# Kernel tuning notes

Measured on AMD Instinct MI355X. Metric: run time of the kernel, lower is better.

The kernel has to match this reference:

```python
import jax, jax.numpy as jnp
import numpy as np

N_NODES = 100000


def _gcn_layer(h_in, W, b, src, dst, norm, num_nodes):
    # PyG GCNConv: linear transform first, then normalized scatter-add aggregation
    h = h_in @ W                                   # [N, out_dim]
    msg = h[src] * norm[:, None]                   # gather + scale over edges
    out = jax.ops.segment_sum(msg, dst, num_segments=num_nodes)
    return out + b


def setup_inputs() -> dict:
    key = jax.random.key(0)
    k1, k2, k3, k4, k5 = jax.random.split(key, 5)
    d_in, d_hid, d_out = 128, 128, 128
    x = jax.random.normal(k1, (N_NODES, d_in), dtype=jnp.float32)
    edge_index = jax.random.randint(k2, (2, 1600000), 0, N_NODES, dtype=jnp.int64)
    # Glorot-ish init for weights, zeros for bias (as in GCNConv defaults)
    W1 = jax.random.normal(k3, (d_in, d_hid), dtype=jnp.float32) / np.sqrt(d_in)
    b1 = jnp.zeros((d_hid,), dtype=jnp.float32)
    W2 = jax.random.normal(k4, (d_hid, d_out), dtype=jnp.float32) / np.sqrt(d_hid)
    b2 = jnp.zeros((d_out,), dtype=jnp.float32)
    return {"x": x, "edge_index": edge_index, "W1": W1, "b1": b1, "W2": W2, "b2": b2}


def reference(x, edge_index, W1, b1, W2, b2):
    num_nodes = x.shape[0]
    # Add self-loops (GCNConv default add_self_loops=True)
    loop = jnp.arange(num_nodes, dtype=edge_index.dtype)
    src = jnp.concatenate([edge_index[0], loop])
    dst = jnp.concatenate([edge_index[1], loop])
    # Symmetric normalization: deg^{-1/2}[src] * deg^{-1/2}[dst]
    deg = jax.ops.segment_sum(jnp.ones_like(dst, dtype=x.dtype), dst, num_segments=num_nodes)
    dinv = jnp.where(deg > 0, jax.lax.rsqrt(deg), 0.0)
    norm = dinv[src] * dinv[dst]                   # [E + N]

    h = _gcn_layer(x, W1, b1, src, dst, norm, num_nodes)
    h = jax.nn.relu(h)                             # dropout is identity in eval mode
    out = _gcn_layer(h, W2, b2, src, dst, norm, num_nodes)
    return out
```

## Files before the change

### kernel.cpp

```cpp
#include <hip/hip_runtime.h>


#define DIM 128
#define CAP 192
typedef unsigned short ushort_t;
typedef unsigned int uint_t;
typedef __attribute__((ext_vector_type(8))) short bf16x8;
typedef __attribute__((ext_vector_type(4))) float f32x4;
typedef __attribute__((ext_vector_type(2))) float f32x2;
typedef __attribute__((ext_vector_type(2))) unsigned int u32x2;

static __device__ __forceinline__ uint_t f2bf(float f) {
    union { float f; uint_t u; } c; c.f = f;
    uint_t u = c.u;
    return (u + 0x7FFFu + ((u >> 16) & 1u)) >> 16;
}
static __device__ __forceinline__ float bf2f(uint_t h) {
    union { uint_t u; float f; } c; c.u = h << 16;
    return c.f;
}
static __device__ __forceinline__ float as_f(uint_t u) {
    union { uint_t u; float f; } c; c.u = u;
    return c.f;
}
static __device__ __forceinline__ void gld16(const void* g, void* l) {
    __builtin_amdgcn_global_load_lds(
        (const __attribute__((address_space(1))) uint_t*)g,
        (__attribute__((address_space(3))) uint_t*)l, 16, 0, 0);
}

__global__ __launch_bounds__(256) void k_bin(const int* __restrict__ src,
                                             const int* __restrict__ dst,
                                             int* __restrict__ bcur,
                                             uint_t* __restrict__ stage,
                                             int E, int RB) {
    int e = blockIdx.x * 256 + threadIdx.x;
    if (e >= E) return;
    int slice = blockIdx.x & 31;
    int s = src[e], d = dst[e];
    int idx = slice * RB + (d >> 7);
    int c = atomicAdd(&bcur[idx], 1);
    if (c < CAP)
        stage[(size_t)idx * CAP + c] = (uint_t)((s << 7) | (d & 127));
}

__global__ __launch_bounds__(1024) void k_bscan(const int* __restrict__ bcur,
                                                int* __restrict__ bbase, int RB) {
    __shared__ int sdat[1024];
    int t = threadIdx.x;
    int v = 0;
    if (t < RB)
        #pragma unroll
        for (int s = 0; s < 32; ++s) v += min(bcur[s * RB + t], CAP);
    sdat[t] = v;
    __syncthreads();
    #pragma unroll
    for (int o = 1; o < 1024; o <<= 1) {
        int x = (t >= o) ? sdat[t - o] : 0;
        __syncthreads();
        sdat[t] += x;
        __syncthreads();
    }
    if (t < RB) bbase[t] = sdat[t] - v;
}

__global__ __launch_bounds__(256) void k_build(const uint_t* __restrict__ stage,
                                               const int* __restrict__ bcur,
                                               const int* __restrict__ bbase,
                                               int* __restrict__ off,
                                               float* __restrict__ dinv,
                                               int* __restrict__ csr_src,
                                               int RB, int N, int E) {
    __shared__ int scnt[33];
    __shared__ int cnt[128], excl[128], lcur[128];
    __shared__ uint_t ent[32 * CAP];
    int b = blockIdx.x, t = threadIdx.x;
    if (t < 32) scnt[t + 1] = min(bcur[t * RB + b], CAP);
    if (t == 0) scnt[0] = 0;
    if (t < 128) { cnt[t] = 0; lcur[t] = 0; }
    __syncthreads();
    if (t == 0)
        for (int s = 1; s <= 32; ++s) scnt[s] += scnt[s - 1];
    __syncthreads();
    int total = scnt[32];
    for (int s = 0; s < 32; ++s) {
        int c0 = scnt[s], c1 = scnt[s + 1];
        const uint_t* sp = stage + (size_t)(s * RB + b) * CAP - c0;
        for (int i = c0 + t; i < c1; i += 256) ent[i] = sp[i];
    }
    __syncthreads();
    for (int i = t; i < total; i += 256) atomicAdd(&cnt[ent[i] & 127], 1);
    __syncthreads();
    if (t < 128) excl[t] = cnt[t];
    __syncthreads();
    #pragma unroll
    for (int o = 1; o < 128; o <<= 1) {
        int x = 0;
        if (t < 128 && t >= o) x = excl[t - o];
        __syncthreads();
        if (t < 128) excl[t] += x;
        __syncthreads();
    }
    int base = bbase[b];
    if (t < 128) {
        excl[t] -= cnt[t];
        int node = (b << 7) + t;
        if (node < N) {
            off[node] = base + excl[t];
            dinv[node] = rsqrtf((float)cnt[t] + 1.0f);
        }
    }
    if (b == RB - 1 && t == 0) off[N] = E;
    __syncthreads();
    for (int i = t; i < total; i += 256) {
        uint_t v = ent[i];
        int dl = v & 127;
        int pos = base + excl[dl] + atomicAdd(&lcur[dl], 1);
        csr_src[pos] = (int)(v >> 7);
    }
}

__global__ __launch_bounds__(256) void k_prep(const float* __restrict__ W1,
                                              const float* __restrict__ W2,
                                              const float* __restrict__ x,
                                              short* __restrict__ whi,
                                              short* __restrict__ wlo,
                                              short* __restrict__ xhi,
                                              short* __restrict__ xlo,
                                              int N, int nxc) {
    int t = threadIdx.x;
    if (blockIdx.x < 16) {
        int g = blockIdx.x * 256 + t;
        int layer = g >> 11, c = g & 2047;
        const float* W = layer ? W2 : W1;
        int ks = c >> 9, nt = (c >> 6) & 7, l = c & 63;
        int q = l >> 4, m = l & 15;
        int n = nt * 16 + m;
        bf16x8 h8, l8;
        #pragma unroll
        for (int j = 0; j < 8; ++j) {
            int k = ks * 32 + q * 8 + j;
            float f = W[k * 128 + n];
            uint_t hb = f2bf(f);
            h8[j] = (short)hb;
            l8[j] = (short)f2bf(f - bf2f(hb));
        }
        ((bf16x8*)whi)[g] = h8;
        ((bf16x8*)wlo)[g] = l8;
    } else {
        int c = (blockIdx.x - 16) * 256 + t;
        if (c >= nxc) return;
        int rb = c >> 11, row = (c >> 4) & 127, cc = c & 15;
        int node = rb * 128 + row;
        bf16x8 h8 = {}, l8 = {};
        if (node < N) {
            f32x4 fa = __builtin_nontemporal_load((const f32x4*)x + node * 32 + cc * 2);
            f32x4 fb = __builtin_nontemporal_load((const f32x4*)x + node * 32 + cc * 2 + 1);
            float f[8] = {fa[0], fa[1], fa[2], fa[3], fb[0], fb[1], fb[2], fb[3]};
            #pragma unroll
            for (int j = 0; j < 8; ++j) {
                uint_t hb = f2bf(f[j]);
                h8[j] = (short)hb;
                l8[j] = (short)f2bf(f[j] - bf2f(hb));
            }
        }
        int slot = rb * 2048 + (cc >> 3) * 1024 + row * 8 + ((cc & 7) ^ (row & 7));
        __builtin_nontemporal_store(h8, (bf16x8*)xhi + slot);
        __builtin_nontemporal_store(l8, (bf16x8*)xlo + slot);
    }
}

__global__ __launch_bounds__(256) void k_gemm(const short* __restrict__ afhi,
                                              const short* __restrict__ aflo,
                                              const short* __restrict__ wfhi,
                                              const short* __restrict__ wflo,
                                              const float* __restrict__ dinv,
                                              ushort_t* __restrict__ hout, int M) {
    __shared__ short AH[8192], AL[8192], WH[8192], WL[8192];
    const int t = threadIdx.x;
    const int rb = blockIdx.x;
    const int wv = t >> 6, l = t & 63;
    const int mb = (wv & 1) * 4;
    const int nbc = (wv >> 1) * 4;

    f32x4 acc[4][4];
    #pragma unroll
    for (int i = 0; i < 4; ++i)
        #pragma unroll
        for (int j = 0; j < 4; ++j)
            acc[i][j] = (f32x4){0.f, 0.f, 0.f, 0.f};

    #pragma unroll
    for (int kc = 0; kc < 2; ++kc) {
        if (kc) __syncthreads();
        {
            const short* ga = afhi + (size_t)rb * 16384 + kc * 8192;
            const short* gb = aflo + (size_t)rb * 16384 + kc * 8192;
            const short* gh = wfhi + kc * 8192;
            const short* gl = wflo + kc * 8192;
            #pragma unroll
            for (int i = 0; i < 4; ++i) {
                int idx = (i * 256 + t) * 8;
                gld16(ga + idx, AH + idx);
                gld16(gb + idx, AL + idx);
                gld16(gh + idx, WH + idx);
                gld16(gl + idx, WL + idx);
            }
        }
        __syncthreads();
        #pragma unroll
        for (int ksl = 0; ksl < 2; ++ksl) {
            bf16x8 ah[4], al[4];
            #pragma unroll
            for (int i = 0; i < 4; ++i) {
                int rowl = (mb + i) * 16 + (l & 15);
                int cA = ksl * 4 + (l >> 4);
                int sa = rowl * 64 + ((cA ^ (rowl & 7)) << 3);
                ah[i] = *(const bf16x8*)&AH[sa];
                al[i] = *(const bf16x8*)&AL[sa];
            }
            #pragma unroll
            for (int j = 0; j < 4; ++j) {
                bf16x8 bh = *(const bf16x8*)&WH[((ksl * 8 + nbc + j) * 64 + l) * 8];
                bf16x8 bl = *(const bf16x8*)&WL[((ksl * 8 + nbc + j) * 64 + l) * 8];
                #pragma unroll
                for (int i = 0; i < 4; ++i) {
                    acc[i][j] = __builtin_amdgcn_mfma_f32_16x16x32_bf16(ah[i], bh, acc[i][j], 0, 0, 0);
                    acc[i][j] = __builtin_amdgcn_mfma_f32_16x16x32_bf16(al[i], bh, acc[i][j], 0, 0, 0);
                    acc[i][j] = __builtin_amdgcn_mfma_f32_16x16x32_bf16(ah[i], bl, acc[i][j], 0, 0, 0);
                }
            }
        }
    }

    const int q = l >> 4, mm = l & 15;
    #pragma unroll
    for (int i = 0; i < 4; ++i)
        #pragma unroll
        for (int r = 0; r < 4; ++r) {
            int gr = rb * 128 + (wv & 1) * 64 + i * 16 + q * 4 + r;
            if (gr < M) {
                float di = dinv[gr];
                #pragma unroll
                for (int j = 0; j < 4; ++j)
                    hout[gr * 128 + nbc * 16 + j * 16 + mm] =
                        (ushort_t)f2bf(di * acc[i][j][r]);
            }
        }
}

template <int NB>
static __device__ __forceinline__ void gbatch(const int* __restrict__ csr,
                                              int e, int half,
                                              const u32x2* __restrict__ hrow,
                                              float& ax, float& ay,
                                              float& az, float& aw) {
    int s[NB]; u32x2 v[NB];
    #pragma unroll
    for (int u = 0; u < NB; ++u)
        s[u] = __builtin_nontemporal_load(&csr[e + 2 * u + half]);
    #pragma unroll
    for (int u = 0; u < NB; ++u) v[u] = hrow[(size_t)s[u] * 32];
    #pragma unroll
    for (int u = 0; u < NB; ++u) {
        ax += as_f(v[u].x << 16); ay += as_f(v[u].x & 0xffff0000u);
        az += as_f(v[u].y << 16); aw += as_f(v[u].y & 0xffff0000u);
    }
}

template <int FRAG>
__global__ __launch_bounds__(256) void k_agg(const uint_t* __restrict__ h32,
                                             const int* __restrict__ off,
                                             const int* __restrict__ csr_src,
                                             const float* __restrict__ dinv,
                                             const float* __restrict__ bias,
                                             float* __restrict__ out,
                                             uint_t* __restrict__ fhi,
                                             uint_t* __restrict__ flo, int N) {
    int n = (blockIdx.x * 256 + threadIdx.x) >> 6;
    if (n >= N) return;
    int l = threadIdx.x & 63;
    int half = l >> 5, c = l & 31;
    const u32x2* hrow = (const u32x2*)h32 + c;

    float ax = 0.f, ay = 0.f, az = 0.f, aw = 0.f;
    if (!half) {
        u32x2 sv = hrow[(size_t)n * 32];
        ax = as_f(sv.x << 16); ay = as_f(sv.x & 0xffff0000u);
        az = as_f(sv.y << 16); aw = as_f(sv.y & 0xffff0000u);
    }

    int e = off[n], end = off[n + 1];
    for (; e + 16 <= end; e += 16) gbatch<8>(csr_src, e, half, hrow, ax, ay, az, aw);
    if (e + 8 <= end) { gbatch<4>(csr_src, e, half, hrow, ax, ay, az, aw); e += 8; }
    if (e + 4 <= end) { gbatch<2>(csr_src, e, half, hrow, ax, ay, az, aw); e += 4; }
    if (e + 2 <= end) { gbatch<1>(csr_src, e, half, hrow, ax, ay, az, aw); e += 2; }
    if (e < end && !half) {
        int s = csr_src[e];
        u32x2 v = hrow[(size_t)s * 32];
        ax += as_f(v.x << 16); ay += as_f(v.x & 0xffff0000u);
        az += as_f(v.y << 16); aw += as_f(v.y & 0xffff0000u);
    }

    ax += __shfl_xor(ax, 32, 64);
    ay += __shfl_xor(ay, 32, 64);
    az += __shfl_xor(az, 32, 64);
    aw += __shfl_xor(aw, 32, 64);
    if (half) return;

    float di = dinv[n];
    f32x4 bv = *((const f32x4*)bias + c);
    ax = di * ax + bv[0];
    ay = di * ay + bv[1];
    az = di * az + bv[2];
    aw = di * aw + bv[3];

    if (FRAG) {
        ax = fmaxf(ax, 0.f); ay = fmaxf(ay, 0.f);
        az = fmaxf(az, 0.f); aw = fmaxf(aw, 0.f);
        uint_t w0h = (f2bf(ay) << 16) | f2bf(ax);
        uint_t w1h = (f2bf(aw) << 16) | f2bf(az);
        uint_t w0l = (f2bf(ay - bf2f(f2bf(ay))) << 16) | f2bf(ax - bf2f(f2bf(ax)));
        uint_t w1l = (f2bf(aw - bf2f(f2bf(aw))) << 16) | f2bf(az - bf2f(f2bf(az)));
        int rb = n >> 7, row = n & 127;
        int p7 = ((c >> 1) & 7) ^ (row & 7);
        size_t i2 = (size_t)rb * 4096 + (c >> 4) * 2048 + row * 16 + p7 * 2 + (c & 1);
        u32x2 vh; vh.x = w0h; vh.y = w1h;
        u32x2 vl; vl.x = w0l; vl.y = w1l;
        __builtin_nontemporal_store(vh, (u32x2*)fhi + i2);
        __builtin_nontemporal_store(vl, (u32x2*)flo + i2);
    } else {
        f32x4 o; o[0] = ax; o[1] = ay; o[2] = az; o[3] = aw;
        __builtin_nontemporal_store(o, (f32x4*)out + (size_t)n * 32 + c);
    }
}

extern "C" void kernel_launch(void* const* d_in, const int* in_sizes, int n_in,
                              void* d_out, int out_size, void* d_ws, size_t ws_size,
                              hipStream_t stream) {
    const float* x  = (const float*)d_in[0];
    const int*   ei = (const int*)d_in[1];
    const float* W1 = (const float*)d_in[2];
    const float* b1 = (const float*)d_in[3];
    const float* W2 = (const float*)d_in[4];
    const float* b2 = (const float*)d_in[5];
    float* out = (float*)d_out;

    const int N = in_sizes[0] / DIM;
    const int E = in_sizes[1] / 2;
    const int* src = ei;
    const int* dst = ei + E;
    const int RB = (N + 127) / 128;
    const int nxc = RB * 2048;

    char* w = (char*)d_ws;
    float* dinv    = (float*)(w);
    int*   bcur    = (int*)  (w + (1 << 19));
    int*   bbase   = (int*)  (w + (1 << 19) + (1 << 17));
    int*   off     = (int*)  (w + (3 << 19));
    short* whi     = (short*)(w + (1 << 21) + (1 << 13));
    short* wlo     = whi + 2 * 16384;
    int*   csr_src = (int*)  (w + ((size_t)5 << 19));
    short* fhi     = (short*)(w + ((size_t)17 << 20));
    short* flo     = (short*)(w + ((size_t)43 << 20));
    ushort_t* hbuf = (ushort_t*)(w + ((size_t)69 << 20));
    uint_t* stage  = (uint_t*)hbuf;

    const int B = 256;
    const int agg_grid = (N * 64 + B - 1) / B;

    hipMemsetAsync(bcur, 0, (size_t)32 * RB * 4, stream);
    k_prep<<<16 + (nxc + B - 1) / B, B, 0, stream>>>(W1, W2, x, whi, wlo,
                                                     fhi, flo, N, nxc);
    k_bin<<<(E + B - 1) / B, B, 0, stream>>>(src, dst, bcur, stage, E, RB);
    k_bscan<<<1, 1024, 0, stream>>>(bcur, bbase, RB);
    k_build<<<RB, B, 0, stream>>>(stage, bcur, bbase, off, dinv, csr_src,
                                  RB, N, E);
    k_gemm<<<RB, B, 0, stream>>>(fhi, flo, whi, wlo, dinv, hbuf, N);
    k_agg<1><<<agg_grid, B, 0, stream>>>((const uint_t*)hbuf, off, csr_src,
                                         dinv, b1, nullptr,
                                         (uint_t*)fhi, (uint_t*)flo, N);
    k_gemm<<<RB, B, 0, stream>>>(fhi, flo, whi + 16384, wlo + 16384, dinv, hbuf, N);
    k_agg<0><<<agg_grid, B, 0, stream>>>((const uint_t*)hbuf, off, csr_src,
                                         dinv, b2, out,
                                         nullptr, nullptr, N);
}
```

Measured before the change: 397.3 us.

## Fuse x bf16 split into first GEMM and drop low part of layer-2 input

The first GEMM now reads fp32 x directly and splits each value into hi/lo bf16 halves as it fills shared memory, so the separate x-conversion pass and its workspace round trip are gone. The layer-1 aggregation stores only the high bf16 half of the ReLU output. The second GEMM therefore loads just that half and skips the lo×W MFMA term. This cuts memory traffic and MFMA work, at the cost of lower precision on the hidden activations feeding layer 2.

```diff
diff --git a/kernel.cpp b/kernel.cpp
--- a/kernel.cpp
+++ b/kernel.cpp
@@ -122,56 +122,30 @@
 
 __global__ __launch_bounds__(256) void k_prep(const float* __restrict__ W1,
                                               const float* __restrict__ W2,
-                                              const float* __restrict__ x,
                                               short* __restrict__ whi,
-                                              short* __restrict__ wlo,
-                                              short* __restrict__ xhi,
-                                              short* __restrict__ xlo,
-                                              int N, int nxc) {
-    int t = threadIdx.x;
-    if (blockIdx.x < 16) {
-        int g = blockIdx.x * 256 + t;
-        int layer = g >> 11, c = g & 2047;
-        const float* W = layer ? W2 : W1;
-        int ks = c >> 9, nt = (c >> 6) & 7, l = c & 63;
-        int q = l >> 4, m = l & 15;
-        int n = nt * 16 + m;
-        bf16x8 h8, l8;
-        #pragma unroll
-        for (int j = 0; j < 8; ++j) {
-            int k = ks * 32 + q * 8 + j;
-            float f = W[k * 128 + n];
-            uint_t hb = f2bf(f);
-            h8[j] = (short)hb;
-            l8[j] = (short)f2bf(f - bf2f(hb));
-        }
-        ((bf16x8*)whi)[g] = h8;
-        ((bf16x8*)wlo)[g] = l8;
-    } else {
-        int c = (blockIdx.x - 16) * 256 + t;
-        if (c >= nxc) return;
-        int rb = c >> 11, row = (c >> 4) & 127, cc = c & 15;
-        int node = rb * 128 + row;
-        bf16x8 h8 = {}, l8 = {};
-        if (node < N) {
-            f32x4 fa = __builtin_nontemporal_load((const f32x4*)x + node * 32 + cc * 2);
-            f32x4 fb = __builtin_nontemporal_load((const f32x4*)x + node * 32 + cc * 2 + 1);
-            float f[8] = {fa[0], fa[1], fa[2], fa[3], fb[0], fb[1], fb[2], fb[3]};
-            #pragma unroll
-            for (int j = 0; j < 8; ++j) {
-                uint_t hb = f2bf(f[j]);
-                h8[j] = (short)hb;
-                l8[j] = (short)f2bf(f[j] - bf2f(hb));
-            }
-        }
-        int slot = rb * 2048 + (cc >> 3) * 1024 + row * 8 + ((cc & 7) ^ (row & 7));
-        __builtin_nontemporal_store(h8, (bf16x8*)xhi + slot);
-        __builtin_nontemporal_store(l8, (bf16x8*)xlo + slot);
-    }
-}
-
+                                              short* __restrict__ wlo) {
+    int g = blockIdx.x * 256 + threadIdx.x;
+    int layer = g >> 11, c = g & 2047;
+    const float* W = layer ? W2 : W1;
+    int ks = c >> 9, nt = (c >> 6) & 7, l = c & 63;
+    int q = l >> 4, m = l & 15;
+    int n = nt * 16 + m;
+    bf16x8 h8, l8;
+    #pragma unroll
+    for (int j = 0; j < 8; ++j) {
+        int k = ks * 32 + q * 8 + j;
+        float f = W[k * 128 + n];
+        uint_t hb = f2bf(f);
+        h8[j] = (short)hb;
+        l8[j] = (short)f2bf(f - bf2f(hb));
+    }
+    ((bf16x8*)whi)[g] = h8;
+    ((bf16x8*)wlo)[g] = l8;
+}
+
+template <int XMODE>
 __global__ __launch_bounds__(256) void k_gemm(const short* __restrict__ afhi,
-                                              const short* __restrict__ aflo,
+                                              const float* __restrict__ xsrc,
                                               const short* __restrict__ wfhi,
                                               const short* __restrict__ wflo,
                                               const float* __restrict__ dinv,
@@ -194,17 +168,45 @@
     for (int kc = 0; kc < 2; ++kc) {
         if (kc) __syncthreads();
         {
-            const short* ga = afhi + (size_t)rb * 16384 + kc * 8192;
-            const short* gb = aflo + (size_t)rb * 16384 + kc * 8192;
             const short* gh = wfhi + kc * 8192;
             const short* gl = wflo + kc * 8192;
+            #pragma unroll
+            for (int i = 0; i < 4; ++i) {
+                int idx = (i * 256 + t) * 8;
+                gld16(gh + idx, WH + idx);
+                gld16(gl + idx, WL + idx);
+            }
+        }
+        if (XMODE == 1) {
+            const short* ga = afhi + (size_t)rb * 16384 + kc * 8192;
             #pragma unroll
             for (int i = 0; i < 4; ++i) {
                 int idx = (i * 256 + t) * 8;
                 gld16(ga + idx, AH + idx);
-                gld16(gb + idx, AL + idx);
-                gld16(gh + idx, WH + idx);
-                gld16(gl + idx, WL + idx);
+            }
+        } else {
+            #pragma unroll
+            for (int i = 0; i < 4; ++i) {
+                int cid = i * 256 + t;
+                int row = cid >> 3, c7 = cid & 7;
+                int node = rb * 128 + row;
+                bf16x8 h8 = {}, l8 = {};
+                if (node < M) {
+                    const float* xp = xsrc + (size_t)node * 128 + kc * 64 + c7 * 8;
+                    f32x4 fa = *(const f32x4*)xp;
+                    f32x4 fb = *(const f32x4*)(xp + 4);
+                    float f[8] = {fa[0], fa[1], fa[2], fa[3],
+                                  fb[0], fb[1], fb[2], fb[3]};
+                    #pragma unroll
+                    for (int j = 0; j < 8; ++j) {
+                        uint_t hb = f2bf(f[j]);
+                        h8[j] = (short)hb;
+                        l8[j] = (short)f2bf(f[j] - bf2f(hb));
+                    }
+                }
+                int dstoff = row * 64 + ((c7 ^ (row & 7)) << 3);
+                *(bf16x8*)&AH[dstoff] = h8;
+                *(bf16x8*)&AL[dstoff] = l8;
             }
         }
         __syncthreads();
@@ -217,7 +219,7 @@
                 int cA = ksl * 4 + (l >> 4);
                 int sa = rowl * 64 + ((cA ^ (rowl & 7)) << 3);
                 ah[i] = *(const bf16x8*)&AH[sa];
-                al[i] = *(const bf16x8*)&AL[sa];
+                if (XMODE == 0) al[i] = *(const bf16x8*)&AL[sa];
             }
             #pragma unroll
             for (int j = 0; j < 4; ++j) {
@@ -226,7 +228,8 @@
                 #pragma unroll
                 for (int i = 0; i < 4; ++i) {
                     acc[i][j] = __builtin_amdgcn_mfma_f32_16x16x32_bf16(ah[i], bh, acc[i][j], 0, 0, 0);
-                    acc[i][j] = __builtin_amdgcn_mfma_f32_16x16x32_bf16(al[i], bh, acc[i][j], 0, 0, 0);
+                    if (XMODE == 0)
+                        acc[i][j] = __builtin_amdgcn_mfma_f32_16x16x32_bf16(al[i], bh, acc[i][j], 0, 0, 0);
                     acc[i][j] = __builtin_amdgcn_mfma_f32_16x16x32_bf16(ah[i], bl, acc[i][j], 0, 0, 0);
                 }
             }
@@ -275,8 +278,7 @@
                                              const float* __restrict__ dinv,
                                              const float* __restrict__ bias,
                                              float* __restrict__ out,
-                                             uint_t* __restrict__ fhi,
-                                             uint_t* __restrict__ flo, int N) {
+                                             uint_t* __restrict__ fhi, int N) {
     int n = (blockIdx.x * 256 + threadIdx.x) >> 6;
     if (n >= N) return;
     int l = threadIdx.x & 63;
@@ -320,15 +322,11 @@
         az = fmaxf(az, 0.f); aw = fmaxf(aw, 0.f);
         uint_t w0h = (f2bf(ay) << 16) | f2bf(ax);
         uint_t w1h = (f2bf(aw) << 16) | f2bf(az);
-        uint_t w0l = (f2bf(ay - bf2f(f2bf(ay))) << 16) | f2bf(ax - bf2f(f2bf(ax)));
-        uint_t w1l = (f2bf(aw - bf2f(f2bf(aw))) << 16) | f2bf(az - bf2f(f2bf(az)));
         int rb = n >> 7, row = n & 127;
         int p7 = ((c >> 1) & 7) ^ (row & 7);
         size_t i2 = (size_t)rb * 4096 + (c >> 4) * 2048 + row * 16 + p7 * 2 + (c & 1);
         u32x2 vh; vh.x = w0h; vh.y = w1h;
-        u32x2 vl; vl.x = w0l; vl.y = w1l;
         __builtin_nontemporal_store(vh, (u32x2*)fhi + i2);
-        __builtin_nontemporal_store(vl, (u32x2*)flo + i2);
     } else {
         f32x4 o; o[0] = ax; o[1] = ay; o[2] = az; o[3] = aw;
         __builtin_nontemporal_store(o, (f32x4*)out + (size_t)n * 32 + c);
@@ -351,7 +349,6 @@
     const int* src = ei;
     const int* dst = ei + E;
     const int RB = (N + 127) / 128;
-    const int nxc = RB * 2048;
 
     char* w = (char*)d_ws;
     float* dinv    = (float*)(w);
@@ -362,7 +359,6 @@
     short* wlo     = whi + 2 * 16384;
     int*   csr_src = (int*)  (w + ((size_t)5 << 19));
     short* fhi     = (short*)(w + ((size_t)17 << 20));
-    short* flo     = (short*)(w + ((size_t)43 << 20));
     ushort_t* hbuf = (ushort_t*)(w + ((size_t)69 << 20));
     uint_t* stage  = (uint_t*)hbuf;
 
@@ -370,18 +366,18 @@
     const int agg_grid = (N * 64 + B - 1) / B;
 
     hipMemsetAsync(bcur, 0, (size_t)32 * RB * 4, stream);
-    k_prep<<<16 + (nxc + B - 1) / B, B, 0, stream>>>(W1, W2, x, whi, wlo,
-                                                     fhi, flo, N, nxc);
+    k_prep<<<16, B, 0, stream>>>(W1, W2, whi, wlo);
     k_bin<<<(E + B - 1) / B, B, 0, stream>>>(src, dst, bcur, stage, E, RB);
     k_bscan<<<1, 1024, 0, stream>>>(bcur, bbase, RB);
     k_build<<<RB, B, 0, stream>>>(stage, bcur, bbase, off, dinv, csr_src,
                                   RB, N, E);
-    k_gemm<<<RB, B, 0, stream>>>(fhi, flo, whi, wlo, dinv, hbuf, N);
+    k_gemm<0><<<RB, B, 0, stream>>>(nullptr, x, whi, wlo, dinv, hbuf, N);
     k_agg<1><<<agg_grid, B, 0, stream>>>((const uint_t*)hbuf, off, csr_src,
                                          dinv, b1, nullptr,
-                                         (uint_t*)fhi, (uint_t*)flo, N);
-    k_gemm<<<RB, B, 0, stream>>>(fhi, flo, whi + 16384, wlo + 16384, dinv, hbuf, N);
+                                         (uint_t*)fhi, N);
+    k_gemm<1><<<RB, B, 0, stream>>>(fhi, nullptr, whi + 16384, wlo + 16384,
+                                    dinv, hbuf, N);
     k_agg<0><<<agg_grid, B, 0, stream>>>((const uint_t*)hbuf, off, csr_src,
                                          dinv, b2, out,
-                                         nullptr, nullptr, N);
-}
+                                         nullptr, N);
+}
```

Result: faster. 375.7 us (-5.4%).
